# Kernel optimization log

Measured on AMD Instinct MI355X. Metric: run time of the kernel, lower is better.

Reference implementation:

```python
import jax, jax.numpy as jnp
import numpy as np

B, M, EMBED, HEADS = 64, 1024, 1024, 8
HD = EMBED // HEADS  # 128
MID = 64             # att_mid_dim[1]
ALPHA = 1.3          # cfg.MODEL.BILINEAR.ELU_ALPHA (CELU)


def celu(x):
    return jax.nn.celu(x, alpha=ALPHA)


def group_norm(x, w, b, G=HEADS, eps=1e-5):
    # torch GroupNorm in source uses unbiased variance (ddof=1)
    N, C = x.shape
    xg = x.reshape(N, G, C // G)
    m = xg.mean(-1, keepdims=True)
    v = xg.var(-1, ddof=1, keepdims=True)
    xg = (xg - m) / jnp.sqrt(v + eps)
    return xg.reshape(N, C) * w + b


def setup_inputs() -> dict:
    key = jax.random.key(0)
    ks = jax.random.split(key, 16)
    s = 0.02
    return {
        "h_state": jax.random.normal(ks[0], (B, EMBED), jnp.float32),
        "att_feats": jax.random.normal(ks[1], (B, M, EMBED), jnp.float32),
        "att_mask": jnp.ones((B, M), jnp.float32),
        "p_att_feats": jax.random.normal(ks[2], (B, M, 2 * EMBED), jnp.float32),
        "Wq": jax.random.normal(ks[3], (EMBED, EMBED), jnp.float32) * s,
        "bq": jnp.zeros((EMBED,), jnp.float32),
        "gnw_q": jnp.ones((EMBED,), jnp.float32),
        "gnb_q": jnp.zeros((EMBED,), jnp.float32),
        "Wv1": jax.random.normal(ks[4], (EMBED, EMBED), jnp.float32) * s,
        "bv1": jnp.zeros((EMBED,), jnp.float32),
        "gnw_v1": jnp.ones((EMBED,), jnp.float32),
        "gnb_v1": jnp.zeros((EMBED,), jnp.float32),
        "Wb": jax.random.normal(ks[5], (HEADS, HD, MID), jnp.float32) * s,
        "bb": jax.random.normal(ks[6], (HEADS, MID), jnp.float32) * s,
        "Ws": jax.random.normal(ks[7], (HEADS, MID, 1), jnp.float32) * s,
        "bs": jax.random.normal(ks[8], (HEADS, 1), jnp.float32) * s,
        "Wc": jax.random.normal(ks[9], (HEADS, MID, HD), jnp.float32) * s,
        "bc": jax.random.normal(ks[10], (HEADS, HD), jnp.float32) * s,
        "Wt": jax.random.normal(ks[11], (2 * EMBED, EMBED), jnp.float32) * s,
        "bt": jnp.zeros((EMBED,), jnp.float32),
        "lnw": jnp.ones((EMBED,), jnp.float32),
        "lnb": jnp.zeros((EMBED,), jnp.float32),
    }


def reference(h_state, att_feats, att_mask, p_att_feats,
              Wq, bq, gnw_q, gnb_q, Wv1, bv1, gnw_v1, gnb_v1,
              Wb, bb, Ws, bs, Wc, bc, Wt, bt, lnw, lnb):
    b = h_state.shape[0]
    # precompute=True path: split p_att_feats into key / value2
    p_key = p_att_feats[..., :EMBED]
    p_value2 = p_att_feats[..., EMBED:]

    # q / v1 branches: Linear -> CELU -> GroupNorm
    q = group_norm(celu(h_state @ Wq + bq), gnw_q, gnb_q)    # [B, E]
    v1 = group_norm(celu(h_state @ Wv1 + bv1), gnw_v1, gnb_v1)

    p_query = q.reshape(b, HEADS, HD)[:, :, None, :]          # [B, H, 1, D]
    p_value1 = v1.reshape(b, HEADS, HD)[:, :, None, :]        # [B, H, 1, D]
    p_key = p_key.reshape(b, M, HEADS, HD).transpose(0, 2, 1, 3)     # [B, H, M, D]
    p_value2 = p_value2.reshape(b, M, HEADS, HD).transpose(0, 2, 1, 3)

    fusion = p_value2 * p_value1                              # [B, H, M, D]
    att_map = p_query * p_key                                 # [B, H, M, D]

    # attention_basic: MH_Linear + ReLU (dropout is identity at eval)
    am = jax.nn.relu(jnp.einsum('bhmi,hio->bhmo', att_map, Wb) + bb[None, :, None, :])  # [B,H,M,MID]

    mask = att_mask[:, None, :]                               # [B, 1, M]
    mext = mask[..., None]                                    # [B, 1, M, 1]
    att_map_pool = (am * mext).sum(-2) / mext.sum(-2)         # [B, H, MID]

    alpha_spatial = (jnp.einsum('bhmi,hio->bhmo', am, Ws) + bs[None, :, None, :])[..., 0]  # [B,H,M]
    alpha_spatial = jnp.where(mask == 0, -1e9, alpha_spatial)
    alpha_spatial = jax.nn.softmax(alpha_spatial, axis=-1)

    att = jnp.einsum('bhm,bhmd->bhd', alpha_spatial, fusion)  # [B, H, D]

    alpha_channel = jax.nn.sigmoid(jnp.einsum('bhi,hio->bho', att_map_pool, Wc) + bc[None])
    att = (att * alpha_channel).reshape(b, EMBED)

    out = jnp.concatenate([h_state, att], axis=-1) @ Wt + bt  # [B, E]
    mu = out.mean(-1, keepdims=True)
    var = out.var(-1, keepdims=True)
    out = (out - mu) / jnp.sqrt(var + 1e-5) * lnw + lnb
    return out
```

## Files before the change

### kernel.cpp

```cpp
#include <hip/hip_runtime.h>
#include <hip/hip_bf16.h>
#include <cmath>

#define NB 64
#define NM 1024
#define NE 1024
#define NH 8
#define NHD 128
#define NMID 64
#define CELU_ALPHA 1.3f

typedef __attribute__((ext_vector_type(8))) short bf16x8;
typedef __attribute__((ext_vector_type(4))) float f32x4;

__device__ __forceinline__ float celuf(float x) {
    return x > 0.f ? x : CELU_ALPHA * expm1f(x / CELU_ALPHA);
}

__device__ __forceinline__ short f2bf(float x) {
    __hip_bfloat16 b = __float2bfloat16(x);
    return *reinterpret_cast<short*>(&b);
}

__global__ __launch_bounds__(256) void a1_tile(
    const float* __restrict__ h, const float* __restrict__ Wq,
    const float* __restrict__ Wv1, float* __restrict__ partA)
{
    const int t = threadIdx.x;
    const int mat = blockIdx.x >> 7;
    const int kq = (blockIdx.x >> 4) & 7;
    const int cc = (blockIdx.x & 15) * 64;
    const int kbase = kq * 128;
    const float* __restrict__ W = mat ? Wv1 : Wq;

    __shared__ float wl[128][64];
    __shared__ float hl[64][132];

#pragma unroll
    for (int u = 0; u < 8; ++u) {
        const int f = t + 256 * u;
        const int row = f >> 4, c4 = f & 15;
        *(float4*)&wl[row][c4 * 4] =
            *(const float4*)&W[(size_t)(kbase + row) * 1024 + cc + c4 * 4];
    }
#pragma unroll
    for (int u = 0; u < 8; ++u) {
        const int f = t + 256 * u;
        const int r = f >> 5, k4 = f & 31;
        *(float4*)&hl[r][k4 * 4] = *(const float4*)&h[r * 1024 + kbase + k4 * 4];
    }
    __syncthreads();

    const int r0 = (t >> 4) * 4;
    const int c0 = (t & 15) * 4;
    float acc[4][4];
#pragma unroll
    for (int i = 0; i < 4; ++i)
#pragma unroll
        for (int j = 0; j < 4; ++j) acc[i][j] = 0.f;

#pragma unroll 4
    for (int k = 0; k < 128; ++k) {
        const float4 w4 = *(const float4*)&wl[k][c0];
        const float h0 = hl[r0][k], h1 = hl[r0 + 1][k];
        const float h2 = hl[r0 + 2][k], h3 = hl[r0 + 3][k];
        acc[0][0] = fmaf(h0, w4.x, acc[0][0]); acc[0][1] = fmaf(h0, w4.y, acc[0][1]);
        acc[0][2] = fmaf(h0, w4.z, acc[0][2]); acc[0][3] = fmaf(h0, w4.w, acc[0][3]);
        acc[1][0] = fmaf(h1, w4.x, acc[1][0]); acc[1][1] = fmaf(h1, w4.y, acc[1][1]);
        acc[1][2] = fmaf(h1, w4.z, acc[1][2]); acc[1][3] = fmaf(h1, w4.w, acc[1][3]);
        acc[2][0] = fmaf(h2, w4.x, acc[2][0]); acc[2][1] = fmaf(h2, w4.y, acc[2][1]);
        acc[2][2] = fmaf(h2, w4.z, acc[2][2]); acc[2][3] = fmaf(h2, w4.w, acc[2][3]);
        acc[3][0] = fmaf(h3, w4.x, acc[3][0]); acc[3][1] = fmaf(h3, w4.y, acc[3][1]);
        acc[3][2] = fmaf(h3, w4.z, acc[3][2]); acc[3][3] = fmaf(h3, w4.w, acc[3][3]);
    }

    float* __restrict__ out = partA + (size_t)(mat * 8 + kq) * 65536;
#pragma unroll
    for (int i = 0; i < 4; ++i) {
        float4 v = {acc[i][0], acc[i][1], acc[i][2], acc[i][3]};
        *(float4*)&out[(r0 + i) * 1024 + cc + c0] = v;
    }
}

__global__ __launch_bounds__(256) void a2b0(
    const float* __restrict__ partA,
    const float* __restrict__ bq, const float* __restrict__ bv1,
    const float* __restrict__ gnw_q, const float* __restrict__ gnb_q,
    const float* __restrict__ gnw_v, const float* __restrict__ gnb_v,
    const float* __restrict__ Wb,
    float* __restrict__ v1buf, short* __restrict__ wbq_g)
{
    const int bid = blockIdx.x;
    const int b = bid >> 3, hh = bid & 7;
    const int t = threadIdx.x;
    const int mat = t >> 7;
    const int c = t & 127;
    const int ch = hh * 128 + c;
    const int w = t >> 6, lane = t & 63;

    __shared__ float q_lds[128];
    __shared__ float red[4][2];

    float x = mat ? bv1[ch] : bq[ch];
#pragma unroll
    for (int kq = 0; kq < 8; ++kq)
        x += partA[(size_t)(mat * 8 + kq) * 65536 + b * 1024 + ch];
    x = celuf(x);

    float s = x, s2 = x * x;
#pragma unroll
    for (int m = 32; m >= 1; m >>= 1) {
        s += __shfl_xor(s, m);
        s2 += __shfl_xor(s2, m);
    }
    if (lane == 0) { red[w][0] = s; red[w][1] = s2; }
    __syncthreads();
    const float S  = red[mat * 2][0] + red[mat * 2 + 1][0];
    const float S2 = red[mat * 2][1] + red[mat * 2 + 1][1];
    const float mean = S * (1.f / 128.f);
    const float var = (S2 - 128.f * mean * mean) * (1.f / 127.f);
    const float inv = rsqrtf(var + 1e-5f);
    const float gw = mat ? gnw_v[ch] : gnw_q[ch];
    const float gb = mat ? gnb_v[ch] : gnb_q[ch];
    const float y = (x - mean) * inv * gw + gb;
    if (mat == 0) q_lds[c] = y;
    else v1buf[b * 1024 + ch] = y;
    __syncthreads();

    const int o = t >> 2;
    const int i0 = (t & 3) * 32;
    union { short sv[32]; uint4 q4[4]; } u;
#pragma unroll 8
    for (int v = 0; v < 32; ++v) {
        const int i = i0 + v;
        u.sv[v] = f2bf(q_lds[i] * Wb[hh * 8192 + i * 64 + o]);
    }
    uint4* dst = (uint4*)&wbq_g[(size_t)bid * 8192 + o * 128 + i0];
#pragma unroll
    for (int r = 0; r < 4; ++r) dst[r] = u.q4[r];
}

__global__ __launch_bounds__(256) void b_fused(
    const float* __restrict__ pat, const float* __restrict__ mask,
    const short* __restrict__ wbq_g,
    const float* __restrict__ bb, const float* __restrict__ Ws,
    const float* __restrict__ bs,
    float* __restrict__ pool_pt, float* __restrict__ esum_pt,
    float* __restrict__ av_pt)
{
    const int t = threadIdx.x;
    const int bid = blockIdx.x;
    const int b = bid >> 5;
    const int h = (bid >> 2) & 7;
    const int chunk = bid & 3;
    const int w = t >> 6;
    const int lane = t & 63;
    const int ln15 = lane & 15;
    const int lg = lane >> 4;
    const int dg = lane & 31;
    const int rwg = lane >> 5;

    __shared__ short wbq_lds[64 * 128];
    __shared__ float mask_lds[256];
    __shared__ float e_lds[4][16];
    __shared__ float att_red[4][128];
    __shared__ float pool_red[4][64];
    __shared__ float esum_red[4];

    mask_lds[t] = mask[b * 1024 + chunk * 256 + t];

    {
        const short* __restrict__ wb = wbq_g + (size_t)(bid >> 2) * 8192;
#pragma unroll
        for (int u = 0; u < 4; ++u) {
            const int f = t + 256 * u;
            const int row = f >> 4, seg = f & 15;
            const int sseg = seg ^ (row & 7);
            *(uint4*)((char*)wbq_lds + row * 256 + sseg * 16) =
                *(const uint4*)(wb + row * 128 + seg * 8);
        }
    }

    float wsr[4], bbr[4];
#pragma unroll
    for (int nt = 0; nt < 4; ++nt) {
        wsr[nt] = Ws[h * 64 + nt * 16 + ln15];
        bbr[nt] = bb[h * 64 + nt * 16 + ln15];
    }
    const float bsh = bs[h];
    float pool_part[4] = {0.f, 0.f, 0.f, 0.f};
    float esum_part = 0.f;
    float4 a4 = {0.f, 0.f, 0.f, 0.f};

    const float* __restrict__ patk = pat + (size_t)b * NM * 2048 + h * 128;
    const float* __restrict__ patv = patk + 1024;

    __syncthreads();

    for (int it = 0; it < 4; ++it) {
        const int ml0 = (w * 4 + it) * 16;
        const int m0 = chunk * 256 + ml0;

        const float* __restrict__ rowp = patk + (size_t)(m0 + ln15) * 2048 + lg * 8;
        float4 ax[4], ay[4];
#pragma unroll
        for (int ks = 0; ks < 4; ++ks) {
            ax[ks] = *(const float4*)(rowp + ks * 32);
            ay[ks] = *(const float4*)(rowp + ks * 32 + 4);
        }

        bf16x8 af[4];
#pragma unroll
        for (int ks = 0; ks < 4; ++ks) {
            union { bf16x8 v; short s[8]; } u8;
            u8.s[0] = f2bf(ax[ks].x); u8.s[1] = f2bf(ax[ks].y);
            u8.s[2] = f2bf(ax[ks].z); u8.s[3] = f2bf(ax[ks].w);
            u8.s[4] = f2bf(ay[ks].x); u8.s[5] = f2bf(ay[ks].y);
            u8.s[6] = f2bf(ay[ks].z); u8.s[7] = f2bf(ay[ks].w);
            af[ks] = u8.v;
        }

        f32x4 acc[4];
#pragma unroll
        for (int nt = 0; nt < 4; ++nt) acc[nt] = (f32x4){0.f, 0.f, 0.f, 0.f};
#pragma unroll
        for (int ks = 0; ks < 4; ++ks) {
            bf16x8 bq[4];
#pragma unroll
            for (int nt = 0; nt < 4; ++nt) {
                const int row = nt * 16 + ln15;
                const int sseg = (ks * 4 + lg) ^ (ln15 & 7);
                bq[nt] = *(const bf16x8*)((const char*)wbq_lds + row * 256 + sseg * 16);
            }
#pragma unroll
            for (int nt = 0; nt < 4; ++nt)
                acc[nt] = __builtin_amdgcn_mfma_f32_16x16x32_bf16(af[ks], bq[nt], acc[nt], 0, 0, 0);
        }

#pragma unroll
        for (int j = 0; j < 4; ++j) {
            const int ml = ml0 + lg * 4 + j;
            const float mk = mask_lds[ml];
            float sp = 0.f;
#pragma unroll
            for (int nt = 0; nt < 4; ++nt) {
                float a = acc[nt][j] + bbr[nt];
                a = fmaxf(a, 0.f);
                sp = fmaf(a, wsr[nt], sp);
                pool_part[nt] = fmaf(a, mk, pool_part[nt]);
            }
            sp += __shfl_xor(sp, 1);
            sp += __shfl_xor(sp, 2);
            sp += __shfl_xor(sp, 4);
            sp += __shfl_xor(sp, 8);
            if (ln15 == 0) {
                const float e = (mk == 0.f) ? 0.f : expf(sp + bsh);
                e_lds[w][lg * 4 + j] = e;
                esum_part += e;
            }
        }

        const float* __restrict__ vrow = patv + (size_t)(m0 + rwg) * 2048 + dg * 4;
#pragma unroll 4
        for (int r = 0; r < 8; ++r) {
            const float4 v = *(const float4*)(vrow + (size_t)(2 * r) * 2048);
            const float e = e_lds[w][rwg + 2 * r];
            a4.x = fmaf(e, v.x, a4.x);
            a4.y = fmaf(e, v.y, a4.y);
            a4.z = fmaf(e, v.z, a4.z);
            a4.w = fmaf(e, v.w, a4.w);
        }
    }

    a4.x += __shfl_xor(a4.x, 32);
    a4.y += __shfl_xor(a4.y, 32);
    a4.z += __shfl_xor(a4.z, 32);
    a4.w += __shfl_xor(a4.w, 32);
    if (lane < 32) *(float4*)&att_red[w][dg * 4] = a4;

#pragma unroll
    for (int nt = 0; nt < 4; ++nt) {
        float p = pool_part[nt];
        p += __shfl_xor(p, 16);
        p += __shfl_xor(p, 32);
        if (lane < 16) pool_red[w][nt * 16 + lane] = p;
    }

#pragma unroll
    for (int m = 32; m >= 1; m >>= 1) esum_part += __shfl_xor(esum_part, m);
    if (lane == 0) esum_red[w] = esum_part;
    __syncthreads();

    if (t < 128)
        av_pt[(size_t)bid * 128 + t] =
            att_red[0][t] + att_red[1][t] + att_red[2][t] + att_red[3][t];
    else if (t < 192)
        pool_pt[(size_t)bid * 64 + (t - 128)] =
            pool_red[0][t - 128] + pool_red[1][t - 128] + pool_red[2][t - 128] + pool_red[3][t - 128];
    else if (t == 192)
        esum_pt[bid] = esum_red[0] + esum_red[1] + esum_red[2] + esum_red[3];
}

__global__ __launch_bounds__(256) void b5_final(
    const float* __restrict__ pool_pt, const float* __restrict__ esum_pt,
    const float* __restrict__ av_pt, const float* __restrict__ mask,
    const float* __restrict__ Wc, const float* __restrict__ bc,
    const float* __restrict__ v1, float* __restrict__ att_out)
{
    const int t = threadIdx.x;
    const int bid = blockIdx.x;
    const int b = bid >> 3;
    const int h = bid & 7;
    const int w = t >> 6, lane = t & 63;

    __shared__ float red4[4];
    __shared__ float pool2[64];

    const float4 mk4 = *(const float4*)&mask[b * 1024 + t * 4];
    float msp = mk4.x + mk4.y + mk4.z + mk4.w;
#pragma unroll
    for (int m = 32; m >= 1; m >>= 1) msp += __shfl_xor(msp, m);
    if (lane == 0) red4[w] = msp;
    __syncthreads();
    const float msum = red4[0] + red4[1] + red4[2] + red4[3];

    if (t < 64) {
        const float pp = pool_pt[(size_t)(bid * 4) * 64 + t] + pool_pt[(size_t)(bid * 4 + 1) * 64 + t]
                       + pool_pt[(size_t)(bid * 4 + 2) * 64 + t] + pool_pt[(size_t)(bid * 4 + 3) * 64 + t];
        pool2[t] = pp / msum;
    }
    __syncthreads();

    if (t < 128) {
        const int d = t;
        const float av = av_pt[(size_t)(bid * 4) * 128 + d] + av_pt[(size_t)(bid * 4 + 1) * 128 + d]
                       + av_pt[(size_t)(bid * 4 + 2) * 128 + d] + av_pt[(size_t)(bid * 4 + 3) * 128 + d];
        const float esum = esum_pt[bid * 4] + esum_pt[bid * 4 + 1]
                         + esum_pt[bid * 4 + 2] + esum_pt[bid * 4 + 3];
        const float att = av / esum;
        float ac = bc[h * 128 + d];
#pragma unroll 8
        for (int o = 0; o < 64; ++o)
            ac = fmaf(pool2[o], Wc[h * 8192 + o * 128 + d], ac);
        const float sig = 1.f / (1.f + expf(-ac));
        att_out[b * 1024 + h * 128 + d] = att * sig * v1[b * 1024 + h * 128 + d];
    }
}

__global__ __launch_bounds__(256) void c1_tile(
    const float* __restrict__ h, const float* __restrict__ att,
    const float* __restrict__ Wt, float* __restrict__ part)
{
    const int t = threadIdx.x;
    const int kq = blockIdx.x >> 4;
    const int cc = (blockIdx.x & 15) * 64;
    const float* __restrict__ x = (kq < 8) ? h : att;
    const int kbase = (kq & 7) * 128;

    __shared__ float wl[128][64];
    __shared__ float hl[64][132];

#pragma unroll
    for (int u = 0; u < 8; ++u) {
        const int f = t + 256 * u;
        const int row = f >> 4, c4 = f & 15;
        *(float4*)&wl[row][c4 * 4] =
            *(const float4*)&Wt[(size_t)(kq * 128 + row) * 1024 + cc + c4 * 4];
    }
#pragma unroll
    for (int u = 0; u < 8; ++u) {
        const int f = t + 256 * u;
        const int r = f >> 5, k4 = f & 31;
        *(float4*)&hl[r][k4 * 4] = *(const float4*)&x[r * 1024 + kbase + k4 * 4];
    }
    __syncthreads();

    const int r0 = (t >> 4) * 4;
    const int c0 = (t & 15) * 4;
    float acc[4][4];
#pragma unroll
    for (int i = 0; i < 4; ++i)
#pragma unroll
        for (int j = 0; j < 4; ++j) acc[i][j] = 0.f;

#pragma unroll 4
    for (int k = 0; k < 128; ++k) {
        const float4 w4 = *(const float4*)&wl[k][c0];
        const float h0 = hl[r0][k], h1 = hl[r0 + 1][k];
        const float h2 = hl[r0 + 2][k], h3 = hl[r0 + 3][k];
        acc[0][0] = fmaf(h0, w4.x, acc[0][0]); acc[0][1] = fmaf(h0, w4.y, acc[0][1]);
        acc[0][2] = fmaf(h0, w4.z, acc[0][2]); acc[0][3] = fmaf(h0, w4.w, acc[0][3]);
        acc[1][0] = fmaf(h1, w4.x, acc[1][0]); acc[1][1] = fmaf(h1, w4.y, acc[1][1]);
        acc[1][2] = fmaf(h1, w4.z, acc[1][2]); acc[1][3] = fmaf(h1, w4.w, acc[1][3]);
        acc[2][0] = fmaf(h2, w4.x, acc[2][0]); acc[2][1] = fmaf(h2, w4.y, acc[2][1]);
        acc[2][2] = fmaf(h2, w4.z, acc[2][2]); acc[2][3] = fmaf(h2, w4.w, acc[2][3]);
        acc[3][0] = fmaf(h3, w4.x, acc[3][0]); acc[3][1] = fmaf(h3, w4.y, acc[3][1]);
        acc[3][2] = fmaf(h3, w4.z, acc[3][2]); acc[3][3] = fmaf(h3, w4.w, acc[3][3]);
    }

#pragma unroll
    for (int i = 0; i < 4; ++i) {
        float4 v = {acc[i][0], acc[i][1], acc[i][2], acc[i][3]};
        *(float4*)&part[(size_t)kq * 65536 + (r0 + i) * 1024 + cc + c0] = v;
    }
}

__global__ __launch_bounds__(256) void c2_ln(
    const float* __restrict__ part, const float* __restrict__ bt,
    const float* __restrict__ lnw, const float* __restrict__ lnb,
    float* __restrict__ out)
{
    const int t = threadIdx.x;
    const int row = blockIdx.x;
    const int w = t >> 6, lane = t & 63;
    __shared__ float red[4];

    float4 v = *(const float4*)&bt[t * 4];
#pragma unroll
    for (int qd = 0; qd < 16; ++qd) {
        const float4 p = *(const float4*)&part[(size_t)qd * 65536 + row * 1024 + t * 4];
        v.x += p.x; v.y += p.y; v.z += p.z; v.w += p.w;
    }
    float s = v.x + v.y + v.z + v.w;
#pragma unroll
    for (int m = 32; m >= 1; m >>= 1) s += __shfl_xor(s, m);
    if (lane == 0) red[w] = s;
    __syncthreads();
    const float mean = (red[0] + red[1] + red[2] + red[3]) * (1.f / 1024.f);
    __syncthreads();
    const float d0 = v.x - mean, d1 = v.y - mean, d2 = v.z - mean, d3 = v.w - mean;
    float ss = d0 * d0 + d1 * d1 + d2 * d2 + d3 * d3;
#pragma unroll
    for (int m = 32; m >= 1; m >>= 1) ss += __shfl_xor(ss, m);
    if (lane == 0) red[w] = ss;
    __syncthreads();
    const float var = (red[0] + red[1] + red[2] + red[3]) * (1.f / 1024.f);
    const float inv = rsqrtf(var + 1e-5f);
    const float4 w4 = *(const float4*)&lnw[t * 4];
    const float4 b4 = *(const float4*)&lnb[t * 4];
    float4 y;
    y.x = d0 * inv * w4.x + b4.x;
    y.y = d1 * inv * w4.y + b4.y;
    y.z = d2 * inv * w4.z + b4.z;
    y.w = d3 * inv * w4.w + b4.w;
    *(float4*)&out[row * 1024 + t * 4] = y;
}

extern "C" void kernel_launch(void* const* d_in, const int* in_sizes, int n_in,
                              void* d_out, int out_size, void* d_ws, size_t ws_size,
                              hipStream_t stream)
{
    const float* h_state  = (const float*)d_in[0];
    const float* att_mask = (const float*)d_in[2];
    const float* pat      = (const float*)d_in[3];
    const float* Wq       = (const float*)d_in[4];
    const float* bq       = (const float*)d_in[5];
    const float* gnw_q    = (const float*)d_in[6];
    const float* gnb_q    = (const float*)d_in[7];
    const float* Wv1      = (const float*)d_in[8];
    const float* bv1      = (const float*)d_in[9];
    const float* gnw_v1   = (const float*)d_in[10];
    const float* gnb_v1   = (const float*)d_in[11];
    const float* Wb       = (const float*)d_in[12];
    const float* bb       = (const float*)d_in[13];
    const float* Ws       = (const float*)d_in[14];
    const float* bs       = (const float*)d_in[15];
    const float* Wc       = (const float*)d_in[16];
    const float* bc       = (const float*)d_in[17];
    const float* Wt       = (const float*)d_in[18];
    const float* bt       = (const float*)d_in[19];
    const float* lnw      = (const float*)d_in[20];
    const float* lnb      = (const float*)d_in[21];
    float* out = (float*)d_out;

    float* ws      = (float*)d_ws;
    float* v1buf   = ws;
    float* attb    = ws + 65536;
    float* parts   = ws + 131072;
    short* wbq_g   = (short*)(ws + 1179648);
    float* pool_pt = ws + 3276800;
    float* esum_pt = ws + 3407872;
    float* av_pt   = ws + 3409920;

    a1_tile<<<256, 256, 0, stream>>>(h_state, Wq, Wv1, parts);
    a2b0<<<512, 256, 0, stream>>>(parts, bq, bv1, gnw_q, gnb_q, gnw_v1, gnb_v1,
                                  Wb, v1buf, wbq_g);
    b_fused<<<2048, 256, 0, stream>>>(pat, att_mask, wbq_g, bb, Ws, bs,
                                      pool_pt, esum_pt, av_pt);
    b5_final<<<512, 256, 0, stream>>>(pool_pt, esum_pt, av_pt, att_mask,
                                      Wc, bc, v1buf, attb);
    c1_tile<<<256, 256, 0, stream>>>(h_state, attb, Wt, parts);
    c2_ln<<<64, 256, 0, stream>>>(parts, bt, lnw, lnb, out);
}
```

Baseline: 162.8 us.

## Fuse channel-attention finalization into output GEMM and stage Wb in LDS

Removes the b5_final kernel. Its channel-gate computation now runs inside the output projection kernel, in the blocks that handle the attention half of K. The mask sum is folded into b_fused's per-chunk reductions, and a2b0 stages Wb through shared memory with a coalesced thread mapping. The intent is to save one launch and the attb round trip. In exchange, every column block for the attention half redundantly recomputes the 64x128 sigmoid gate (64-wide dot products), and c1 uses more LDS.

```diff
diff --git a/kernel.cpp b/kernel.cpp
--- a/kernel.cpp
+++ b/kernel.cpp
@@ -100,6 +100,14 @@
 
     __shared__ float q_lds[128];
     __shared__ float red[4][2];
+    __shared__ float wb_l[128][68];
+
+#pragma unroll
+    for (int u = 0; u < 8; ++u) {
+        const int f = t + 256 * u;
+        const int i = f >> 4, o4 = f & 15;
+        *(float4*)&wb_l[i][o4 * 4] = *(const float4*)&Wb[hh * 8192 + i * 64 + o4 * 4];
+    }
 
     float x = mat ? bv1[ch] : bq[ch];
 #pragma unroll
@@ -127,13 +135,13 @@
     else v1buf[b * 1024 + ch] = y;
     __syncthreads();
 
-    const int o = t >> 2;
-    const int i0 = (t & 3) * 32;
+    const int o = t & 63;
+    const int i0 = (t >> 6) * 32;
     union { short sv[32]; uint4 q4[4]; } u;
 #pragma unroll 8
     for (int v = 0; v < 32; ++v) {
         const int i = i0 + v;
-        u.sv[v] = f2bf(q_lds[i] * Wb[hh * 8192 + i * 64 + o]);
+        u.sv[v] = f2bf(q_lds[i] * wb_l[i][o]);
     }
     uint4* dst = (uint4*)&wbq_g[(size_t)bid * 8192 + o * 128 + i0];
 #pragma unroll
@@ -146,7 +154,7 @@
     const float* __restrict__ bb, const float* __restrict__ Ws,
     const float* __restrict__ bs,
     float* __restrict__ pool_pt, float* __restrict__ esum_pt,
-    float* __restrict__ av_pt)
+    float* __restrict__ msum_pt, float* __restrict__ av_pt)
 {
     const int t = threadIdx.x;
     const int bid = blockIdx.x;
@@ -166,8 +174,16 @@
     __shared__ float att_red[4][128];
     __shared__ float pool_red[4][64];
     __shared__ float esum_red[4];
-
-    mask_lds[t] = mask[b * 1024 + chunk * 256 + t];
+    __shared__ float msum_red[4];
+
+    const float mk0 = mask[b * 1024 + chunk * 256 + t];
+    mask_lds[t] = mk0;
+    {
+        float msp = mk0;
+#pragma unroll
+        for (int m = 32; m >= 1; m >>= 1) msp += __shfl_xor(msp, m);
+        if (lane == 0) msum_red[w] = msp;
+    }
 
     {
         const short* __restrict__ wb = wbq_g + (size_t)(bid >> 2) * 8192;
@@ -299,66 +315,77 @@
             pool_red[0][t - 128] + pool_red[1][t - 128] + pool_red[2][t - 128] + pool_red[3][t - 128];
     else if (t == 192)
         esum_pt[bid] = esum_red[0] + esum_red[1] + esum_red[2] + esum_red[3];
-}
-
-__global__ __launch_bounds__(256) void b5_final(
+    else if (t == 193)
+        msum_pt[bid] = msum_red[0] + msum_red[1] + msum_red[2] + msum_red[3];
+}
+
+__global__ __launch_bounds__(256) void c1_fused(
+    const float* __restrict__ h, const float* __restrict__ Wt,
     const float* __restrict__ pool_pt, const float* __restrict__ esum_pt,
-    const float* __restrict__ av_pt, const float* __restrict__ mask,
+    const float* __restrict__ msum_pt, const float* __restrict__ av_pt,
     const float* __restrict__ Wc, const float* __restrict__ bc,
-    const float* __restrict__ v1, float* __restrict__ att_out)
-{
-    const int t = threadIdx.x;
-    const int bid = blockIdx.x;
-    const int b = bid >> 3;
-    const int h = bid & 7;
-    const int w = t >> 6, lane = t & 63;
-
-    __shared__ float red4[4];
-    __shared__ float pool2[64];
-
-    const float4 mk4 = *(const float4*)&mask[b * 1024 + t * 4];
-    float msp = mk4.x + mk4.y + mk4.z + mk4.w;
-#pragma unroll
-    for (int m = 32; m >= 1; m >>= 1) msp += __shfl_xor(msp, m);
-    if (lane == 0) red4[w] = msp;
-    __syncthreads();
-    const float msum = red4[0] + red4[1] + red4[2] + red4[3];
-
-    if (t < 64) {
-        const float pp = pool_pt[(size_t)(bid * 4) * 64 + t] + pool_pt[(size_t)(bid * 4 + 1) * 64 + t]
-                       + pool_pt[(size_t)(bid * 4 + 2) * 64 + t] + pool_pt[(size_t)(bid * 4 + 3) * 64 + t];
-        pool2[t] = pp / msum;
-    }
-    __syncthreads();
-
-    if (t < 128) {
-        const int d = t;
-        const float av = av_pt[(size_t)(bid * 4) * 128 + d] + av_pt[(size_t)(bid * 4 + 1) * 128 + d]
-                       + av_pt[(size_t)(bid * 4 + 2) * 128 + d] + av_pt[(size_t)(bid * 4 + 3) * 128 + d];
-        const float esum = esum_pt[bid * 4] + esum_pt[bid * 4 + 1]
-                         + esum_pt[bid * 4 + 2] + esum_pt[bid * 4 + 3];
-        const float att = av / esum;
-        float ac = bc[h * 128 + d];
-#pragma unroll 8
-        for (int o = 0; o < 64; ++o)
-            ac = fmaf(pool2[o], Wc[h * 8192 + o * 128 + d], ac);
-        const float sig = 1.f / (1.f + expf(-ac));
-        att_out[b * 1024 + h * 128 + d] = att * sig * v1[b * 1024 + h * 128 + d];
-    }
-}
-
-__global__ __launch_bounds__(256) void c1_tile(
-    const float* __restrict__ h, const float* __restrict__ att,
-    const float* __restrict__ Wt, float* __restrict__ part)
+    const float* __restrict__ v1, float* __restrict__ part)
 {
     const int t = threadIdx.x;
     const int kq = blockIdx.x >> 4;
     const int cc = (blockIdx.x & 15) * 64;
-    const float* __restrict__ x = (kq < 8) ? h : att;
-    const int kbase = (kq & 7) * 128;
 
     __shared__ float wl[128][64];
-    __shared__ float hl[64][132];
+    __shared__ float xl[64][132];
+    __shared__ float pool2_l[64][64];
+    __shared__ float esum_l[64];
+    __shared__ float msum_l[64];
+
+    float (*wc_l)[128] = (float(*)[128])wl;
+
+    if (kq >= 8) {
+        const int hh = kq & 7;
+#pragma unroll
+        for (int u = 0; u < 8; ++u) {
+            const int f = t + 256 * u;
+            const int o = f >> 5, d4 = f & 31;
+            *(float4*)&wc_l[o][d4 * 4] = *(const float4*)&Wc[hh * 8192 + o * 128 + d4 * 4];
+        }
+        if (t < 64) {
+            const int b = t;
+            const size_t base = (size_t)(b * 8 + hh) * 4;
+            esum_l[b] = esum_pt[base] + esum_pt[base + 1] + esum_pt[base + 2] + esum_pt[base + 3];
+            msum_l[b] = msum_pt[base] + msum_pt[base + 1] + msum_pt[base + 2] + msum_pt[base + 3];
+        }
+        __syncthreads();
+#pragma unroll
+        for (int u = 0; u < 16; ++u) {
+            const int f = t + 256 * u;
+            const int b = f >> 6, o = f & 63;
+            const size_t base = ((size_t)(b * 8 + hh) * 4) * 64 + o;
+            pool2_l[b][o] = (pool_pt[base] + pool_pt[base + 64]
+                           + pool_pt[base + 128] + pool_pt[base + 192]) / msum_l[b];
+        }
+        __syncthreads();
+#pragma unroll
+        for (int u = 0; u < 32; ++u) {
+            const int f = t + 256 * u;
+            const int b = f >> 7, d = f & 127;
+            const size_t base = ((size_t)(b * 8 + hh) * 4) * 128 + d;
+            const float av = av_pt[base] + av_pt[base + 128]
+                           + av_pt[base + 256] + av_pt[base + 384];
+            float ac = bc[hh * 128 + d];
+#pragma unroll 8
+            for (int o = 0; o < 64; ++o)
+                ac = fmaf(pool2_l[b][o], wc_l[o][d], ac);
+            const float sig = 1.f / (1.f + expf(-ac));
+            xl[b][d] = (av / esum_l[b]) * sig * v1[b * 1024 + hh * 128 + d];
+        }
+        __syncthreads();
+    } else {
+        const int kbase = kq * 128;
+#pragma unroll
+        for (int u = 0; u < 8; ++u) {
+            const int f = t + 256 * u;
+            const int r = f >> 5, k4 = f & 31;
+            *(float4*)&xl[r][k4 * 4] = *(const float4*)&h[r * 1024 + kbase + k4 * 4];
+        }
+    }
 
 #pragma unroll
     for (int u = 0; u < 8; ++u) {
@@ -367,12 +394,6 @@
         *(float4*)&wl[row][c4 * 4] =
             *(const float4*)&Wt[(size_t)(kq * 128 + row) * 1024 + cc + c4 * 4];
     }
-#pragma unroll
-    for (int u = 0; u < 8; ++u) {
-        const int f = t + 256 * u;
-        const int r = f >> 5, k4 = f & 31;
-        *(float4*)&hl[r][k4 * 4] = *(const float4*)&x[r * 1024 + kbase + k4 * 4];
-    }
     __syncthreads();
 
     const int r0 = (t >> 4) * 4;
@@ -386,8 +407,8 @@
 #pragma unroll 4
     for (int k = 0; k < 128; ++k) {
         const float4 w4 = *(const float4*)&wl[k][c0];
-        const float h0 = hl[r0][k], h1 = hl[r0 + 1][k];
-        const float h2 = hl[r0 + 2][k], h3 = hl[r0 + 3][k];
+        const float h0 = xl[r0][k], h1 = xl[r0 + 1][k];
+        const float h2 = xl[r0 + 2][k], h3 = xl[r0 + 3][k];
         acc[0][0] = fmaf(h0, w4.x, acc[0][0]); acc[0][1] = fmaf(h0, w4.y, acc[0][1]);
         acc[0][2] = fmaf(h0, w4.z, acc[0][2]); acc[0][3] = fmaf(h0, w4.w, acc[0][3]);
         acc[1][0] = fmaf(h1, w4.x, acc[1][0]); acc[1][1] = fmaf(h1, w4.y, acc[1][1]);
@@ -475,20 +496,19 @@
 
     float* ws      = (float*)d_ws;
     float* v1buf   = ws;
-    float* attb    = ws + 65536;
-    float* parts   = ws + 131072;
-    short* wbq_g   = (short*)(ws + 1179648);
-    float* pool_pt = ws + 3276800;
-    float* esum_pt = ws + 3407872;
-    float* av_pt   = ws + 3409920;
+    float* parts   = ws + 65536;
+    short* wbq_g   = (short*)(ws + 1114112);
+    float* pool_pt = ws + 3211264;
+    float* esum_pt = ws + 3342336;
+    float* msum_pt = ws + 3344384;
+    float* av_pt   = ws + 3346432;
 
     a1_tile<<<256, 256, 0, stream>>>(h_state, Wq, Wv1, parts);
     a2b0<<<512, 256, 0, stream>>>(parts, bq, bv1, gnw_q, gnb_q, gnw_v1, gnb_v1,
                                   Wb, v1buf, wbq_g);
     b_fused<<<2048, 256, 0, stream>>>(pat, att_mask, wbq_g, bb, Ws, bs,
-                                      pool_pt, esum_pt, av_pt);
-    b5_final<<<512, 256, 0, stream>>>(pool_pt, esum_pt, av_pt, att_mask,
-                                      Wc, bc, v1buf, attb);
-    c1_tile<<<256, 256, 0, stream>>>(h_state, attb, Wt, parts);
+                                      pool_pt, esum_pt, msum_pt, av_pt);
+    c1_fused<<<256, 256, 0, stream>>>(h_state, Wt, pool_pt, esum_pt, msum_pt,
+                                      av_pt, Wc, bc, v1buf, parts);
     c2_ln<<<64, 256, 0, stream>>>(parts, bt, lnw, lnb, out);
 }
```

Measured after the change: 172.3 us. 1.06x slower.
